# Kernel optimization log

Hardware: AMD Instinct MI355X
Metric: run time of the kernel (lower is better)

Reference implementation:

```python
import jax, jax.numpy as jnp
import numpy as np

D_MODEL = 1024
N_HEADS = 16
D_HEAD = D_MODEL // N_HEADS  # 64
D_FF = D_MODEL  # FeedForward(d_model, d_model) in source
B, S = 4, 1024
EPS = 1e-5


def layer_norm(x, gamma, beta):
    mu = jnp.mean(x, axis=-1, keepdims=True)
    var = jnp.mean(jnp.square(x - mu), axis=-1, keepdims=True)
    return (x - mu) * jax.lax.rsqrt(var + EPS) * gamma + beta


def setup_inputs() -> dict:
    key = jax.random.key(0)
    ks = jax.random.split(key, 16)
    s_embed = 1.0 / np.sqrt(D_MODEL)
    s_ff = 1.0 / np.sqrt(D_FF)
    return {
        "x": jax.random.normal(ks[0], (B, S, D_MODEL), jnp.float32),
        # per-head QKV projections stacked over heads: [H, d_embed, d_head]
        "Wq": jax.random.normal(ks[1], (N_HEADS, D_MODEL, D_HEAD), jnp.float32) * s_embed,
        "bq": jax.random.normal(ks[2], (N_HEADS, D_HEAD), jnp.float32) * s_embed,
        "Wk": jax.random.normal(ks[3], (N_HEADS, D_MODEL, D_HEAD), jnp.float32) * s_embed,
        "bk": jax.random.normal(ks[4], (N_HEADS, D_HEAD), jnp.float32) * s_embed,
        "Wv": jax.random.normal(ks[5], (N_HEADS, D_MODEL, D_HEAD), jnp.float32) * s_embed,
        "bv": jax.random.normal(ks[6], (N_HEADS, D_HEAD), jnp.float32) * s_embed,
        "Wo": jax.random.normal(ks[7], (D_MODEL, D_MODEL), jnp.float32) * s_embed,
        "bo": jax.random.normal(ks[8], (D_MODEL,), jnp.float32) * s_embed,
        "g1": jnp.ones((D_MODEL,), jnp.float32),
        "be1": jnp.zeros((D_MODEL,), jnp.float32),
        "W1": jax.random.normal(ks[9], (D_MODEL, D_FF), jnp.float32) * s_embed,
        "b1": jax.random.normal(ks[10], (D_FF,), jnp.float32) * s_embed,
        "W2": jax.random.normal(ks[11], (D_FF, D_MODEL), jnp.float32) * s_ff,
        "b2": jax.random.normal(ks[12], (D_MODEL,), jnp.float32) * s_ff,
        "g2": jnp.ones((D_MODEL,), jnp.float32),
        "be2": jnp.zeros((D_MODEL,), jnp.float32),
    }


def reference(x, Wq, bq, Wk, bk, Wv, bv, Wo, bo, g1, be1, W1, b1, W2, b2, g2, be2):
    scale = 1.0 / np.sqrt(D_HEAD).astype(np.float32)
    # batched per-head projections (equivalent to the per-head Linear loop)
    Q = jnp.einsum('bse,hed->bhsd', x, Wq) + bq[None, :, None, :]
    K = jnp.einsum('bse,hed->bhsd', x, Wk) + bk[None, :, None, :]
    V = jnp.einsum('bse,hed->bhsd', x, Wv) + bv[None, :, None, :]
    scores = jnp.einsum('bhsd,bhtd->bhst', Q, K) * scale
    attn = jax.nn.softmax(scores, axis=-1)
    ctx = jnp.einsum('bhst,bhtd->bhsd', attn, V)
    # concat heads along feature dim (head order matches the torch cat)
    ctx = jnp.transpose(ctx, (0, 2, 1, 3)).reshape(x.shape[0], x.shape[1], D_MODEL)
    attn_out = ctx @ Wo + bo
    y1 = layer_norm(x + attn_out, g1, be1)
    ff = jax.nn.relu(y1 @ W1 + b1) @ W2 + b2  # dropout is identity in eval
    return layer_norm(y1 + ff, g2, be2)
```

## Files before the change

kernel.cpp:

```cpp
#include <hip/hip_runtime.h>
#include <stdint.h>

#define BSZ 4
#define SEQ 1024
#define DM 1024
#define NH 16
#define DH 64
#define ROWS (BSZ * SEQ)
#define QS3 3072

typedef unsigned short u16;
typedef short bf16x8 __attribute__((ext_vector_type(8)));
typedef float f32x4 __attribute__((ext_vector_type(4)));

__device__ __forceinline__ float b2f(u16 u) {
    union { uint32_t i; float f; } v; v.i = ((uint32_t)u) << 16; return v.f;
}
__device__ __forceinline__ u16 f2b(float f) {
    union { float f; uint32_t i; } v; v.f = f;
    uint32_t u = v.i;
    return (u16)((u + 0x7FFFu + ((u >> 16) & 1u)) >> 16);
}
__device__ __forceinline__ u16 f2b_rh(float f) {
    union { float f; uint32_t i; } v; v.f = f;
    return (u16)((v.i + 0x8000u) >> 16);
}

__device__ __forceinline__ size_t blk_idx(int row, int col, int nkt) {
    return (((size_t)((row >> 7) * nkt + (col >> 5))) << 12)
         + ((((row >> 4) & 7) * 64 + ((col >> 3) & 3) * 16 + (row & 15)) << 3)
         + (col & 7);
}

typedef const __attribute__((address_space(1))) void gv_t;
typedef __attribute__((address_space(3))) void lv_t;
__device__ __forceinline__ void gl_lds16(const void* g, void* l) {
    __builtin_amdgcn_global_load_lds((gv_t*)g, (lv_t*)l, 16, 0, 0);
}

__global__ __launch_bounds__(256) void detect_dtype(
    const uint32_t* __restrict__ x, int* __restrict__ flag)
{
    __shared__ int red[256];
    const int tid = threadIdx.x;
    int sane = 0;
    for (int i = tid; i < 1024; i += 256) {
        uint32_t w = x[i];
        uint32_t lo = w & 0xFFFFu;
        uint32_t e = (lo >> 7) & 0xFF;
        if ((e >= 100 && e <= 140) || lo == 0) sane++;
    }
    red[tid] = sane;
    __syncthreads();
    for (int st = 128; st > 0; st >>= 1) {
        if (tid < st) red[tid] += red[tid + st];
        __syncthreads();
    }
    if (tid == 0) flag[0] = (red[0] < 512) ? 1 : 0;
}

__global__ __launch_bounds__(256) void convert_vecs(
    const void* bq, const void* bk, const void* bv, const void* bo,
    const void* b1, const void* b2, const void* g1, const void* be1,
    const void* g2, const void* be2, u16* __restrict__ dst,
    const int* __restrict__ flag)
{
    int i = blockIdx.x * 256 + threadIdx.x;
    int seg = i >> 10, off = i & 1023;
    const void* srcs[10] = {bq, bk, bv, bo, b1, b2, g1, be1, g2, be2};
    const void* s = srcs[seg];
    if (flag[0]) dst[i] = f2b(((const float*)s)[off]);
    else         dst[i] = ((const u16*)s)[off];
}

__global__ __launch_bounds__(256) void convert_x_blocked(
    const void* __restrict__ src, u16* __restrict__ dst,
    const int* __restrict__ flag)
{
    const int gid = blockIdx.x * 256 + threadIdx.x;
    const int tile = gid >> 9, c = gid & 511;
    const int p = tile >> 5, t = tile & 31;
    const int r = p * 128 + ((c >> 6) & 7) * 16 + (c & 15);
    const int k = t * 32 + ((c >> 4) & 3) * 8;
    union { uint4 q; u16 s[8]; } o;
    if (flag[0]) {
        const float* s = (const float*)src + (size_t)r * DM + k;
        float4 f0 = *(const float4*)s;
        float4 f1 = *(const float4*)(s + 4);
        o.s[0] = f2b(f0.x); o.s[1] = f2b(f0.y); o.s[2] = f2b(f0.z); o.s[3] = f2b(f0.w);
        o.s[4] = f2b(f1.x); o.s[5] = f2b(f1.y); o.s[6] = f2b(f1.z); o.s[7] = f2b(f1.w);
    } else {
        o.q = *(const uint4*)((const u16*)src + (size_t)r * DM + k);
    }
    *(uint4*)&dst[(size_t)gid * 8] = o.q;
}

__global__ __launch_bounds__(256) void transpose_blocked(
    const void* __restrict__ src, u16* __restrict__ dst, int R, int C,
    int n_off, const int* __restrict__ flag)
{
    __shared__ u16 Ts[32][33];
    const int tid = threadIdx.x;
    const int cb = blockIdx.x * 32, rb = blockIdx.y * 32, z = blockIdx.z;
    const int tr = tid >> 3, tc4 = (tid & 7) * 4;
    const size_t sbase = (size_t)z * R * C;

    u16 v[4];
    if (flag[0]) {
        const float* s = (const float*)src + sbase + (size_t)(rb + tr) * C + cb + tc4;
        float4 f = *(const float4*)s;
        v[0] = f2b(f.x); v[1] = f2b(f.y); v[2] = f2b(f.z); v[3] = f2b(f.w);
    } else {
        const u16* s = (const u16*)src + sbase + (size_t)(rb + tr) * C + cb + tc4;
        ushort4 f = *(const ushort4*)s;
        v[0] = f.x; v[1] = f.y; v[2] = f.z; v[3] = f.w;
    }
    #pragma unroll
    for (int j = 0; j < 4; ++j) Ts[tc4 + j][tr] = v[j];
    __syncthreads();

    if (tid < 128) {
        const int np = tid & 31, qp = tid >> 5;
        const int n = n_off + z * C + cb + np;
        const int k = rb + qp * 8;
        union { uint4 q; u16 s[8]; } o;
        #pragma unroll
        for (int j = 0; j < 8; ++j) o.s[j] = Ts[np][qp * 8 + j];
        *(uint4*)&dst[blk_idx(n, k, 32)] = o.q;
    }
}

__global__ __launch_bounds__(256) void gemm_b128(
    const u16* __restrict__ Ab, const u16* __restrict__ Bb,
    const u16* __restrict__ bias, const u16* __restrict__ resid,
    u16* __restrict__ C, int M, int N, int K,
    int relu, int c_blocked, int resid_blocked)
{
    __shared__ uint4 smem4[2176];
    u16* As = (u16*)smem4;
    u16* Bs = (u16*)smem4 + 8192;
    u16* Cs = (u16*)smem4;

    const int tid = threadIdx.x;
    const int w = tid >> 6, lane = tid & 63;
    const int l16 = lane & 15, quad = lane >> 4;
    const int wr = w >> 1, wc = w & 1;
    const int bm = blockIdx.y * 128, bn = blockIdx.x * 128;
    const int nkt = K >> 5;

    const u16* At = Ab + ((size_t)(bm >> 7) * nkt << 12);
    const u16* Bt = Bb + ((size_t)(bn >> 7) * nkt << 12);

    f32x4 acc[4][4];
    #pragma unroll
    for (int i = 0; i < 4; ++i)
        #pragma unroll
        for (int j = 0; j < 4; ++j)
            acc[i][j] = (f32x4){0.f, 0.f, 0.f, 0.f};

    const int co0 = (w * 64) * 8, co1 = (256 + w * 64) * 8;

    gl_lds16(&At[(size_t)0 + (w * 64 + lane) * 8],         &As[co0]);
    gl_lds16(&At[(size_t)0 + (256 + w * 64 + lane) * 8],   &As[co1]);
    gl_lds16(&Bt[(size_t)0 + (w * 64 + lane) * 8],         &Bs[co0]);
    gl_lds16(&Bt[(size_t)0 + (256 + w * 64 + lane) * 8],   &Bs[co1]);
    __syncthreads();

    for (int kt = 0; kt < nkt; ++kt) {
        const int cur = (kt & 1) * 4096, nxt = cur ^ 4096;
        if (kt + 1 < nkt) {
            const size_t tb = (size_t)(kt + 1) << 12;
            gl_lds16(&At[tb + (w * 64 + lane) * 8],       &As[nxt + co0]);
            gl_lds16(&At[tb + (256 + w * 64 + lane) * 8], &As[nxt + co1]);
            gl_lds16(&Bt[tb + (w * 64 + lane) * 8],       &Bs[nxt + co0]);
            gl_lds16(&Bt[tb + (256 + w * 64 + lane) * 8], &Bs[nxt + co1]);
        }

        bf16x8 a[4], b[4];
        #pragma unroll
        for (int i = 0; i < 4; ++i)
            a[i] = *(const bf16x8*)&As[cur + (((wr * 4 + i) * 64) + quad * 16 + l16) * 8];
        #pragma unroll
        for (int j = 0; j < 4; ++j)
            b[j] = *(const bf16x8*)&Bs[cur + (((wc * 4 + j) * 64) + quad * 16 + l16) * 8];

        #pragma unroll
        for (int i = 0; i < 4; ++i)
            #pragma unroll
            for (int j = 0; j < 4; ++j)
                acc[i][j] = __builtin_amdgcn_mfma_f32_16x16x32_bf16(a[i], b[j], acc[i][j], 0, 0, 0);
        __syncthreads();
    }

    #pragma unroll
    for (int j = 0; j < 4; ++j) {
        const int lc = wc * 64 + j * 16 + l16;
        const int col = bn + lc;
        const float bj = bias ? b2f(bias[col]) : 0.f;
        #pragma unroll
        for (int i = 0; i < 4; ++i) {
            #pragma unroll
            for (int r = 0; r < 4; ++r) {
                const int lr = wr * 64 + i * 16 + quad * 4 + r;
                float v = acc[i][j][r] + bj;
                if (resid) {
                    const size_t ri = resid_blocked ? blk_idx(bm + lr, col, N >> 5)
                                                    : (size_t)(bm + lr) * N + col;
                    v += b2f(resid[ri]);
                }
                if (relu) v = v > 0.f ? v : 0.f;
                Cs[lr * 136 + lc] = f2b(v);
            }
        }
    }
    __syncthreads();

    if (!c_blocked) {
        #pragma unroll
        for (int u = 0; u < 8; ++u) {
            const int g = u * 256 + tid;
            const int row = g >> 4, c16 = g & 15;
            uint4 val = *(const uint4*)&Cs[row * 136 + c16 * 8];
            *(uint4*)&C[(size_t)(bm + row) * N + bn + c16 * 8] = val;
        }
    } else {
        const size_t obase = ((size_t)((bm >> 7) * (N >> 5) + (bn >> 5))) << 12;
        #pragma unroll
        for (int u = 0; u < 8; ++u) {
            const int cc = u * 256 + tid;
            const int t2 = cc >> 9, c = cc & 511;
            const int row = ((c >> 6) & 7) * 16 + (c & 15);
            const int col = t2 * 32 + ((c >> 4) & 3) * 8;
            uint4 val = *(const uint4*)&Cs[row * 136 + col];
            *(uint4*)&C[obase + ((size_t)t2 << 12) + (size_t)c * 8] = val;
        }
    }
}

__global__ __launch_bounds__(256) void gemm_b64(
    const u16* __restrict__ Ab, const u16* __restrict__ Bb,
    const u16* __restrict__ bias, const u16* __restrict__ resid,
    u16* __restrict__ C, int M, int N, int K,
    int relu, int c_blocked, int resid_blocked)
{
    __shared__ uint4 smem4[1536];
    u16* As = (u16*)smem4;
    u16* Bs = (u16*)smem4 + 8192;
    u16* Cs = (u16*)smem4;

    const int tid = threadIdx.x;
    const int w = tid >> 6, lane = tid & 63;
    const int l16 = lane & 15, quad = lane >> 4;
    const int bm = blockIdx.y * 128, bn = blockIdx.x * 64;
    const int nkt = K >> 5;

    const u16* At = Ab + ((size_t)(bm >> 7) * nkt << 12);
    const int bsub = ((bn >> 6) & 1) * 256;
    const u16* Bt = Bb + ((size_t)(bn >> 7) * nkt << 12);

    f32x4 acc[2][4];
    #pragma unroll
    for (int i = 0; i < 2; ++i)
        #pragma unroll
        for (int j = 0; j < 4; ++j)
            acc[i][j] = (f32x4){0.f, 0.f, 0.f, 0.f};

    const int co0 = (w * 64) * 8, co1 = (256 + w * 64) * 8;

    gl_lds16(&At[(size_t)0 + (w * 64 + lane) * 8],       &As[co0]);
    gl_lds16(&At[(size_t)0 + (256 + w * 64 + lane) * 8], &As[co1]);
    gl_lds16(&Bt[(size_t)0 + (bsub + w * 64 + lane) * 8], &Bs[co0]);
    __syncthreads();

    for (int kt = 0; kt < nkt; ++kt) {
        const int curA = (kt & 1) * 4096, nxtA = curA ^ 4096;
        const int curB = (kt & 1) * 2048, nxtB = curB ^ 2048;
        if (kt + 1 < nkt) {
            const size_t tb = (size_t)(kt + 1) << 12;
            gl_lds16(&At[tb + (w * 64 + lane) * 8],        &As[nxtA + co0]);
            gl_lds16(&At[tb + (256 + w * 64 + lane) * 8],  &As[nxtA + co1]);
            gl_lds16(&Bt[tb + (bsub + w * 64 + lane) * 8], &Bs[nxtB + co0]);
        }

        bf16x8 a[2], b[4];
        #pragma unroll
        for (int i = 0; i < 2; ++i)
            a[i] = *(const bf16x8*)&As[curA + (((w * 2 + i) * 64) + quad * 16 + l16) * 8];
        #pragma unroll
        for (int j = 0; j < 4; ++j)
            b[j] = *(const bf16x8*)&Bs[curB + ((j * 64) + quad * 16 + l16) * 8];

        #pragma unroll
        for (int i = 0; i < 2; ++i)
            #pragma unroll
            for (int j = 0; j < 4; ++j)
                acc[i][j] = __builtin_amdgcn_mfma_f32_16x16x32_bf16(a[i], b[j], acc[i][j], 0, 0, 0);
        __syncthreads();
    }

    #pragma unroll
    for (int j = 0; j < 4; ++j) {
        const int lc = j * 16 + l16;
        const int col = bn + lc;
        const float bj = bias ? b2f(bias[col]) : 0.f;
        #pragma unroll
        for (int i = 0; i < 2; ++i) {
            #pragma unroll
            for (int r = 0; r < 4; ++r) {
                const int lr = w * 32 + i * 16 + quad * 4 + r;
                float v = acc[i][j][r] + bj;
                if (resid) {
                    const size_t ri = resid_blocked ? blk_idx(bm + lr, col, N >> 5)
                                                    : (size_t)(bm + lr) * N + col;
                    v += b2f(resid[ri]);
                }
                if (relu) v = v > 0.f ? v : 0.f;
                Cs[lr * 72 + lc] = f2b(v);
            }
        }
    }
    __syncthreads();

    if (!c_blocked) {
        #pragma unroll
        for (int u = 0; u < 4; ++u) {
            const int g = u * 256 + tid;
            const int row = g >> 3, c16 = g & 7;
            uint4 val = *(const uint4*)&Cs[row * 72 + c16 * 8];
            *(uint4*)&C[(size_t)(bm + row) * N + bn + c16 * 8] = val;
        }
    } else {
        const size_t obase = ((size_t)((bm >> 7) * (N >> 5) + (bn >> 5))) << 12;
        #pragma unroll
        for (int u = 0; u < 4; ++u) {
            const int cc = u * 256 + tid;
            const int t2 = cc >> 9, c = cc & 511;
            const int row = ((c >> 6) & 7) * 16 + (c & 15);
            const int col = t2 * 32 + ((c >> 4) & 3) * 8;
            uint4 val = *(const uint4*)&Cs[row * 72 + col];
            *(uint4*)&C[obase + ((size_t)t2 << 12) + (size_t)c * 8] = val;
        }
    }
}

__global__ __launch_bounds__(512) void attn_mfma(
    const u16* __restrict__ QKV, u16* __restrict__ ctx)
{
    __shared__ u16 Qf[8192];
    __shared__ u16 Kf[2][4096];
    __shared__ u16 VtT[2][64 * 72];
    __shared__ u16 Ps[8 * 16 * 72];

    const int qt = blockIdx.x, h = blockIdx.y, b = blockIdx.z;
    const int tid = threadIdx.x;
    const int w = tid >> 6, lane = tid & 63;
    const int l16 = lane & 15, quad = lane >> 4;
    const size_t qrow0 = (size_t)(b * SEQ + qt * 128);
    const size_t brow = (size_t)(b * SEQ);
    const int hoff = h * DH;

    const size_t qg = (qrow0 + w * 16 + l16) * QS3 + hoff + quad * 8;
    gl_lds16(&QKV[qg],      &Qf[w * 1024]);
    gl_lds16(&QKV[qg + 32], &Qf[w * 1024 + 512]);

    const int kt_ = w >> 1, kh_ = w & 1;
    const size_t kgbase = (size_t)(kt_ * 16 + l16) * QS3 + 1024 + hoff + kh_ * 32 + quad * 8;
    const int kdst = kt_ * 1024 + kh_ * 512;

    const int vk2 = (tid & 31) * 2, vd0 = (tid >> 5) * 4;
    const size_t vgbase = (size_t)vk2 * QS3 + 2048 + hoff + vd0;

    gl_lds16(&QKV[brow * QS3 + kgbase], &Kf[0][kdst]);
    {
        uint2 a0 = *(const uint2*)&QKV[brow * QS3 + vgbase];
        uint2 a1 = *(const uint2*)&QKV[brow * QS3 + vgbase + QS3];
        uint32_t w0 = (a0.x & 0xFFFFu) | (a1.x << 16);
        uint32_t w1 = (a0.x >> 16)     | (a1.x & 0xFFFF0000u);
        uint32_t w2 = (a0.y & 0xFFFFu) | (a1.y << 16);
        uint32_t w3 = (a0.y >> 16)     | (a1.y & 0xFFFF0000u);
        *(uint32_t*)&VtT[0][(vd0 + 0) * 72 + vk2] = w0;
        *(uint32_t*)&VtT[0][(vd0 + 1) * 72 + vk2] = w1;
        *(uint32_t*)&VtT[0][(vd0 + 2) * 72 + vk2] = w2;
        *(uint32_t*)&VtT[0][(vd0 + 3) * 72 + vk2] = w3;
    }
    __syncthreads();

    bf16x8 aQ0 = *(const bf16x8*)&Qf[w * 1024 +       lane * 8];
    bf16x8 aQ1 = *(const bf16x8*)&Qf[w * 1024 + 512 + lane * 8];

    f32x4 O[4];
    #pragma unroll
    for (int dt = 0; dt < 4; ++dt) O[dt] = (f32x4){0.f, 0.f, 0.f, 0.f};
    float lacc[4] = {0.f, 0.f, 0.f, 0.f};

    for (int kt64 = 0; kt64 < SEQ / 64; ++kt64) {
        const int cur = kt64 & 1, nxt = cur ^ 1;
        uint2 a0, a1;
        const bool more = (kt64 + 1 < SEQ / 64);
        if (more) {
            const size_t krow = brow + (size_t)(kt64 + 1) * 64;
            gl_lds16(&QKV[krow * QS3 + kgbase], &Kf[nxt][kdst]);
            a0 = *(const uint2*)&QKV[krow * QS3 + vgbase];
            a1 = *(const uint2*)&QKV[krow * QS3 + vgbase + QS3];
        }

        f32x4 St[4];
        #pragma unroll
        for (int t = 0; t < 4; ++t) {
            bf16x8 b0 = *(const bf16x8*)&Kf[cur][t * 1024 +       lane * 8];
            bf16x8 b1 = *(const bf16x8*)&Kf[cur][t * 1024 + 512 + lane * 8];
            f32x4 z = (f32x4){0.f, 0.f, 0.f, 0.f};
            z = __builtin_amdgcn_mfma_f32_16x16x32_bf16(aQ0, b0, z, 0, 0, 0);
            z = __builtin_amdgcn_mfma_f32_16x16x32_bf16(aQ1, b1, z, 0, 0, 0);
            St[t] = z;
        }

        #pragma unroll
        for (int t = 0; t < 4; ++t)
            #pragma unroll
            for (int r = 0; r < 4; ++r) {
                const float p = __expf(St[t][r] * 0.125f);
                lacc[r] += p;
                Ps[w * 1152 + (quad * 4 + r) * 72 + t * 16 + l16] = f2b_rh(p);
            }

        bf16x8 aP0 = *(const bf16x8*)&Ps[w * 1152 + l16 * 72 +  0 + quad * 8];
        bf16x8 aP1 = *(const bf16x8*)&Ps[w * 1152 + l16 * 72 + 32 + quad * 8];
        #pragma unroll
        for (int dt = 0; dt < 4; ++dt) {
            bf16x8 vv0 = *(const bf16x8*)&VtT[cur][(dt * 16 + l16) * 72 +  0 + quad * 8];
            bf16x8 vv1 = *(const bf16x8*)&VtT[cur][(dt * 16 + l16) * 72 + 32 + quad * 8];
            O[dt] = __builtin_amdgcn_mfma_f32_16x16x32_bf16(aP0, vv0, O[dt], 0, 0, 0);
            O[dt] = __builtin_amdgcn_mfma_f32_16x16x32_bf16(aP1, vv1, O[dt], 0, 0, 0);
        }

        if (more) {
            uint32_t w0 = (a0.x & 0xFFFFu) | (a1.x << 16);
            uint32_t w1 = (a0.x >> 16)     | (a1.x & 0xFFFF0000u);
            uint32_t w2 = (a0.y & 0xFFFFu) | (a1.y << 16);
            uint32_t w3 = (a0.y >> 16)     | (a1.y & 0xFFFF0000u);
            *(uint32_t*)&VtT[nxt][(vd0 + 0) * 72 + vk2] = w0;
            *(uint32_t*)&VtT[nxt][(vd0 + 1) * 72 + vk2] = w1;
            *(uint32_t*)&VtT[nxt][(vd0 + 2) * 72 + vk2] = w2;
            *(uint32_t*)&VtT[nxt][(vd0 + 3) * 72 + vk2] = w3;
        }
        __syncthreads();
    }

    const size_t pbase = ((size_t)(qrow0 >> 7) * 32) << 12;
    #pragma unroll
    for (int r = 0; r < 4; ++r) {
        float s = lacc[r];
        s += __shfl_xor(s, 1);
        s += __shfl_xor(s, 2);
        s += __shfl_xor(s, 4);
        s += __shfl_xor(s, 8);
        const float inv = 1.0f / s;
        #pragma unroll
        for (int dt = 0; dt < 4; ++dt) {
            const int t = h * 2 + (dt >> 1);
            const int q = (dt & 1) * 2 + (l16 >> 3);
            const size_t idx = pbase + ((size_t)t << 12)
                             + ((w * 64 + q * 16 + quad * 4 + r) << 3) + (l16 & 7);
            ctx[idx] = f2b(O[dt][r] * inv);
        }
    }
}

__global__ __launch_bounds__(256) void layernorm_kernel(
    const u16* __restrict__ X, const u16* __restrict__ gamma,
    const u16* __restrict__ beta, void* __restrict__ Y,
    const int* __restrict__ flag, int y_mode)
{
    __shared__ float red[256], red2[256];
    const int r = blockIdx.x, tid = threadIdx.x;
    const u16* xp = X + (size_t)r * DM;

    ushort4 v = *(const ushort4*)(xp + tid * 4);
    float x0 = b2f(v.x), x1 = b2f(v.y), x2 = b2f(v.z), x3 = b2f(v.w);
    red[tid]  = x0 + x1 + x2 + x3;
    red2[tid] = x0 * x0 + x1 * x1 + x2 * x2 + x3 * x3;
    __syncthreads();
    for (int st = 128; st > 0; st >>= 1) {
        if (tid < st) { red[tid] += red[tid + st]; red2[tid] += red2[tid + st]; }
        __syncthreads();
    }
    const float mu = red[0] * (1.0f / DM);
    const float var = red2[0] * (1.0f / DM) - mu * mu;
    const float rstd = rsqrtf(var + 1e-5f);

    ushort4 g = *(const ushort4*)(gamma + tid * 4);
    ushort4 be = *(const ushort4*)(beta + tid * 4);
    float y0 = (x0 - mu) * rstd * b2f(g.x) + b2f(be.x);
    float y1 = (x1 - mu) * rstd * b2f(g.y) + b2f(be.y);
    float y2 = (x2 - mu) * rstd * b2f(g.z) + b2f(be.z);
    float y3 = (x3 - mu) * rstd * b2f(g.w) + b2f(be.w);

    const int k = tid * 4;
    if (y_mode == 2 && flag[0]) {
        float* yp = (float*)Y + (size_t)r * DM + k;
        yp[0] = y0; yp[1] = y1; yp[2] = y2; yp[3] = y3;
    } else if (y_mode == 1) {
        u16* yp = (u16*)Y + blk_idx(r, k, 32);
        ushort4 o; o.x = f2b(y0); o.y = f2b(y1); o.z = f2b(y2); o.w = f2b(y3);
        *(ushort4*)yp = o;
    } else {
        u16* yp = (u16*)Y + (size_t)r * DM + k;
        ushort4 o; o.x = f2b(y0); o.y = f2b(y1); o.z = f2b(y2); o.w = f2b(y3);
        *(ushort4*)yp = o;
    }
}

extern "C" void kernel_launch(void* const* d_in, const int* in_sizes, int n_in,
                              void* d_out, int out_size, void* d_ws, size_t ws_size,
                              hipStream_t stream) {
    const void* x_raw   = d_in[0];
    const void* Wq_raw  = d_in[1];
    const void* bq_raw  = d_in[2];
    const void* Wk_raw  = d_in[3];
    const void* bk_raw  = d_in[4];
    const void* Wv_raw  = d_in[5];
    const void* bv_raw  = d_in[6];
    const void* Wo_raw  = d_in[7];
    const void* bo_raw  = d_in[8];
    const void* g1_raw  = d_in[9];
    const void* be1_raw = d_in[10];
    const void* W1_raw  = d_in[11];
    const void* b1_raw  = d_in[12];
    const void* W2_raw  = d_in[13];
    const void* b2_raw  = d_in[14];
    const void* g2_raw  = d_in[15];
    const void* be2_raw = d_in[16];

    char* ws = (char*)d_ws;
    const size_t MB = 1024 * 1024;
    int* flag   = (int*)ws;
    u16* x_b    = (u16*)(ws + 1 * MB);
    u16* WqkvB  = (u16*)(ws + 9 * MB);
    u16* WoB    = (u16*)(ws + 15 * MB);
    u16* W1B    = (u16*)(ws + 17 * MB);
    u16* W2B    = (u16*)(ws + 19 * MB);
    u16* vecs   = (u16*)(ws + 21 * MB);
    u16* bqkv_c = vecs;
    u16* bo_c   = vecs + 3072;
    u16* b1_c   = vecs + 4096;
    u16* b2_c   = vecs + 5120;
    u16* g1_c   = vecs + 6144;
    u16* be1_c  = vecs + 7168;
    u16* g2_c   = vecs + 8192;
    u16* be2_c  = vecs + 9216;
    u16* QKVb   = (u16*)(ws + 22 * MB);
    u16* y1B    = QKVb;
    u16* hmidB  = QKVb + 4 * MB;
    u16* ctxB   = (u16*)(ws + 48 * MB);
    u16* res1   = (u16*)(ws + 56 * MB);
    u16* res2   = res1;

    detect_dtype<<<1, 256, 0, stream>>>((const uint32_t*)x_raw, flag);

    convert_x_blocked<<<2048, 256, 0, stream>>>(x_raw, x_b, flag);

    dim3 gt_qkv(2, 32, NH);
    transpose_blocked<<<gt_qkv, 256, 0, stream>>>(Wq_raw, WqkvB, DM, DH,    0, flag);
    transpose_blocked<<<gt_qkv, 256, 0, stream>>>(Wk_raw, WqkvB, DM, DH, 1024, flag);
    transpose_blocked<<<gt_qkv, 256, 0, stream>>>(Wv_raw, WqkvB, DM, DH, 2048, flag);
    dim3 gt_sq(32, 32, 1);
    transpose_blocked<<<gt_sq, 256, 0, stream>>>(Wo_raw, WoB, DM, DM, 0, flag);
    transpose_blocked<<<gt_sq, 256, 0, stream>>>(W1_raw, W1B, DM, DM, 0, flag);
    transpose_blocked<<<gt_sq, 256, 0, stream>>>(W2_raw, W2B, DM, DM, 0, flag);

    convert_vecs<<<40, 256, 0, stream>>>(bq_raw, bk_raw, bv_raw, bo_raw,
                                         b1_raw, b2_raw, g1_raw, be1_raw,
                                         g2_raw, be2_raw, vecs, flag);

    gemm_b128<<<dim3(QS3 / 128, ROWS / 128), 256, 0, stream>>>(
        x_b, WqkvB, bqkv_c, nullptr, QKVb, ROWS, QS3, DM, 0, 0, 0);

    attn_mfma<<<dim3(SEQ / 128, NH, BSZ), 512, 0, stream>>>(QKVb, ctxB);

    dim3 gg64(DM / 64, ROWS / 128);
    gemm_b64<<<gg64, 256, 0, stream>>>(ctxB, WoB, bo_c, x_b, res1, ROWS, DM, DM, 0, 0, 1);
    layernorm_kernel<<<ROWS, 256, 0, stream>>>(res1, g1_c, be1_c, (void*)y1B, flag, 1);
    gemm_b64<<<gg64, 256, 0, stream>>>(y1B, W1B, b1_c, nullptr, hmidB, ROWS, DM, DM, 1, 1, 0);
    gemm_b64<<<gg64, 256, 0, stream>>>(hmidB, W2B, b2_c, y1B, res2, ROWS, DM, DM, 0, 0, 1);
    layernorm_kernel<<<ROWS, 256, 0, stream>>>(res2, g2_c, be2_c, d_out, flag, 2);
}
```

Before: 277.5 us.

## Write QKV in attention-ready blocked layouts and merge prep kernels into one launch

The QKV GEMM epilogue now writes Q, K and V straight into per-head blocked layouts, with V pre-transposed, so the attention kernel can stage K and V tiles into LDS with direct global-to-LDS copies. This removes the in-kernel V transpose and the strided row loads. The dtype conversion, weight transpose and vector conversion kernels are also merged into a single prep_all launch to cut launch overhead. In exchange the GEMM epilogue does scattered LDS reads for the V transpose, and the attention context output indexing changes.

```diff
diff --git a/kernel.cpp b/kernel.cpp
--- a/kernel.cpp
+++ b/kernel.cpp
@@ -59,54 +59,70 @@
     if (tid == 0) flag[0] = (red[0] < 512) ? 1 : 0;
 }
 
-__global__ __launch_bounds__(256) void convert_vecs(
+__global__ __launch_bounds__(256) void prep_all(
+    const void* x_raw, const void* Wq, const void* Wk, const void* Wv,
+    const void* Wo, const void* W1, const void* W2,
     const void* bq, const void* bk, const void* bv, const void* bo,
     const void* b1, const void* b2, const void* g1, const void* be1,
-    const void* g2, const void* be2, u16* __restrict__ dst,
+    const void* g2, const void* be2,
+    u16* __restrict__ x_b, u16* __restrict__ WqkvB, u16* __restrict__ WoB,
+    u16* __restrict__ W1B, u16* __restrict__ W2B, u16* __restrict__ vecs,
     const int* __restrict__ flag)
 {
-    int i = blockIdx.x * 256 + threadIdx.x;
-    int seg = i >> 10, off = i & 1023;
-    const void* srcs[10] = {bq, bk, bv, bo, b1, b2, g1, be1, g2, be2};
-    const void* s = srcs[seg];
-    if (flag[0]) dst[i] = f2b(((const float*)s)[off]);
-    else         dst[i] = ((const u16*)s)[off];
-}
-
-__global__ __launch_bounds__(256) void convert_x_blocked(
-    const void* __restrict__ src, u16* __restrict__ dst,
-    const int* __restrict__ flag)
-{
-    const int gid = blockIdx.x * 256 + threadIdx.x;
-    const int tile = gid >> 9, c = gid & 511;
-    const int p = tile >> 5, t = tile & 31;
-    const int r = p * 128 + ((c >> 6) & 7) * 16 + (c & 15);
-    const int k = t * 32 + ((c >> 4) & 3) * 8;
-    union { uint4 q; u16 s[8]; } o;
-    if (flag[0]) {
-        const float* s = (const float*)src + (size_t)r * DM + k;
-        float4 f0 = *(const float4*)s;
-        float4 f1 = *(const float4*)(s + 4);
-        o.s[0] = f2b(f0.x); o.s[1] = f2b(f0.y); o.s[2] = f2b(f0.z); o.s[3] = f2b(f0.w);
-        o.s[4] = f2b(f1.x); o.s[5] = f2b(f1.y); o.s[6] = f2b(f1.z); o.s[7] = f2b(f1.w);
+    const int bid = blockIdx.x, tid = threadIdx.x;
+    const int isf = flag[0];
+
+    if (bid < 2048) {
+        const int gid = bid * 256 + tid;
+        const int tile = gid >> 9, c = gid & 511;
+        const int p = tile >> 5, t = tile & 31;
+        const int r = p * 128 + ((c >> 6) & 7) * 16 + (c & 15);
+        const int k = t * 32 + ((c >> 4) & 3) * 8;
+        union { uint4 q; u16 s[8]; } o;
+        if (isf) {
+            const float* s = (const float*)x_raw + (size_t)r * DM + k;
+            float4 f0 = *(const float4*)s;
+            float4 f1 = *(const float4*)(s + 4);
+            o.s[0] = f2b(f0.x); o.s[1] = f2b(f0.y); o.s[2] = f2b(f0.z); o.s[3] = f2b(f0.w);
+            o.s[4] = f2b(f1.x); o.s[5] = f2b(f1.y); o.s[6] = f2b(f1.z); o.s[7] = f2b(f1.w);
+        } else {
+            o.q = *(const uint4*)((const u16*)x_raw + (size_t)r * DM + k);
+        }
+        *(uint4*)&x_b[(size_t)gid * 8] = o.q;
+        return;
+    }
+    if (bid >= 8192) {
+        const int i = (bid - 8192) * 256 + tid;
+        const int seg = i >> 10, off = i & 1023;
+        const void* srcs[10] = {bq, bk, bv, bo, b1, b2, g1, be1, g2, be2};
+        const void* s = srcs[seg];
+        vecs[i] = isf ? f2b(((const float*)s)[off]) : ((const u16*)s)[off];
+        return;
+    }
+
+    const void* src; u16* dst; int R, C, n_off, bx, by, z;
+    if (bid < 5120) {
+        const int which = (bid - 2048) >> 10;
+        const int lb = (bid - 2048) & 1023;
+        src = which == 0 ? Wq : (which == 1 ? Wk : Wv);
+        dst = WqkvB; R = DM; C = DH; n_off = which * 1024;
+        bx = lb & 1; by = (lb >> 1) & 31; z = lb >> 6;
     } else {
-        o.q = *(const uint4*)((const u16*)src + (size_t)r * DM + k);
-    }
-    *(uint4*)&dst[(size_t)gid * 8] = o.q;
-}
-
-__global__ __launch_bounds__(256) void transpose_blocked(
-    const void* __restrict__ src, u16* __restrict__ dst, int R, int C,
-    int n_off, const int* __restrict__ flag)
-{
+        const int which = (bid - 5120) >> 10;
+        const int lb = (bid - 5120) & 1023;
+        src = which == 0 ? Wo : (which == 1 ? W1 : W2);
+        dst = which == 0 ? WoB : (which == 1 ? W1B : W2B);
+        R = DM; C = DM; n_off = 0;
+        bx = lb & 31; by = (lb >> 5) & 31; z = 0;
+    }
+
     __shared__ u16 Ts[32][33];
-    const int tid = threadIdx.x;
-    const int cb = blockIdx.x * 32, rb = blockIdx.y * 32, z = blockIdx.z;
+    const int cb = bx * 32, rb = by * 32;
     const int tr = tid >> 3, tc4 = (tid & 7) * 4;
     const size_t sbase = (size_t)z * R * C;
 
     u16 v[4];
-    if (flag[0]) {
+    if (isf) {
         const float* s = (const float*)src + sbase + (size_t)(rb + tr) * C + cb + tc4;
         float4 f = *(const float4*)s;
         v[0] = f2b(f.x); v[1] = f2b(f.y); v[2] = f2b(f.z); v[3] = f2b(f.w);
@@ -130,11 +146,10 @@
     }
 }
 
-__global__ __launch_bounds__(256) void gemm_b128(
+__global__ __launch_bounds__(256) void gemm_qkv(
     const u16* __restrict__ Ab, const u16* __restrict__ Bb,
-    const u16* __restrict__ bias, const u16* __restrict__ resid,
-    u16* __restrict__ C, int M, int N, int K,
-    int relu, int c_blocked, int resid_blocked)
+    const u16* __restrict__ bias,
+    u16* __restrict__ Qblk, u16* __restrict__ Kblk, u16* __restrict__ Vblk)
 {
     __shared__ uint4 smem4[2176];
     u16* As = (u16*)smem4;
@@ -146,7 +161,7 @@
     const int l16 = lane & 15, quad = lane >> 4;
     const int wr = w >> 1, wc = w & 1;
     const int bm = blockIdx.y * 128, bn = blockIdx.x * 128;
-    const int nkt = K >> 5;
+    const int nkt = 32;
 
     const u16* At = Ab + ((size_t)(bm >> 7) * nkt << 12);
     const u16* Bt = Bb + ((size_t)(bn >> 7) * nkt << 12);
@@ -160,10 +175,10 @@
 
     const int co0 = (w * 64) * 8, co1 = (256 + w * 64) * 8;
 
-    gl_lds16(&At[(size_t)0 + (w * 64 + lane) * 8],         &As[co0]);
-    gl_lds16(&At[(size_t)0 + (256 + w * 64 + lane) * 8],   &As[co1]);
-    gl_lds16(&Bt[(size_t)0 + (w * 64 + lane) * 8],         &Bs[co0]);
-    gl_lds16(&Bt[(size_t)0 + (256 + w * 64 + lane) * 8],   &Bs[co1]);
+    gl_lds16(&At[(w * 64 + lane) * 8],         &As[co0]);
+    gl_lds16(&At[(256 + w * 64 + lane) * 8],   &As[co1]);
+    gl_lds16(&Bt[(w * 64 + lane) * 8],         &Bs[co0]);
+    gl_lds16(&Bt[(256 + w * 64 + lane) * 8],   &Bs[co1]);
     __syncthreads();
 
     for (int kt = 0; kt < nkt; ++kt) {
@@ -195,44 +210,50 @@
     #pragma unroll
     for (int j = 0; j < 4; ++j) {
         const int lc = wc * 64 + j * 16 + l16;
-        const int col = bn + lc;
-        const float bj = bias ? b2f(bias[col]) : 0.f;
-        #pragma unroll
-        for (int i = 0; i < 4; ++i) {
+        const float bj = b2f(bias[bn + lc]);
+        #pragma unroll
+        for (int i = 0; i < 4; ++i)
             #pragma unroll
             for (int r = 0; r < 4; ++r) {
                 const int lr = wr * 64 + i * 16 + quad * 4 + r;
-                float v = acc[i][j][r] + bj;
-                if (resid) {
-                    const size_t ri = resid_blocked ? blk_idx(bm + lr, col, N >> 5)
-                                                    : (size_t)(bm + lr) * N + col;
-                    v += b2f(resid[ri]);
-                }
-                if (relu) v = v > 0.f ? v : 0.f;
-                Cs[lr * 136 + lc] = f2b(v);
+                Cs[lr * 136 + lc] = f2b(acc[i][j][r] + bj);
             }
-        }
-    }
-    __syncthreads();
-
-    if (!c_blocked) {
+    }
+    __syncthreads();
+
+    const int b_ = bm >> 10, sb16 = (bm & 1023) >> 4, kb64 = (bm & 1023) >> 6;
+    if (bn < 2048) {
+        u16* out = (bn < 1024) ? Qblk : Kblk;
+        const int hbase = (bn & 1023) >> 6;
         #pragma unroll
         for (int u = 0; u < 8; ++u) {
             const int g = u * 256 + tid;
-            const int row = g >> 4, c16 = g & 15;
-            uint4 val = *(const uint4*)&Cs[row * 136 + c16 * 8];
-            *(uint4*)&C[(size_t)(bm + row) * N + bn + c16 * 8] = val;
+            const int hh = g >> 10, rem = g & 1023;
+            const int s16r = rem >> 7, rem2 = rem & 127;
+            const int half = rem2 >> 6, lam = rem2 & 63;
+            const int row = s16r * 16 + (lam & 15);
+            const int col = hh * 64 + half * 32 + (lam >> 4) * 8;
+            uint4 val = *(const uint4*)&Cs[row * 136 + col];
+            const size_t gi = ((size_t)((b_ * 16 + hbase + hh) * 64 + sb16 + s16r)) * 1024
+                            + half * 512 + (size_t)lam * 8;
+            *(uint4*)&out[gi] = val;
         }
     } else {
-        const size_t obase = ((size_t)((bm >> 7) * (N >> 5) + (bn >> 5))) << 12;
+        const int hbase = (bn - 2048) >> 6;
         #pragma unroll
         for (int u = 0; u < 8; ++u) {
-            const int cc = u * 256 + tid;
-            const int t2 = cc >> 9, c = cc & 511;
-            const int row = ((c >> 6) & 7) * 16 + (c & 15);
-            const int col = t2 * 32 + ((c >> 4) & 3) * 8;
-            uint4 val = *(const uint4*)&Cs[row * 136 + col];
-            *(uint4*)&C[obase + ((size_t)t2 << 12) + (size_t)c * 8] = val;
+            const int g = u * 256 + tid;
+            const int hh = g >> 10, rem = g & 1023;
+            const int kt64r = rem >> 9, dt = (rem >> 7) & 3;
+            const int half = (rem >> 6) & 1, lam = rem & 63;
+            const int d = dt * 16 + (lam & 15);
+            const int s0 = kt64r * 64 + half * 32 + (lam >> 4) * 8;
+            union { uint4 q; u16 s[8]; } o;
+            #pragma unroll
+            for (int j = 0; j < 8; ++j) o.s[j] = Cs[(s0 + j) * 136 + hh * 64 + d];
+            const size_t gi = ((size_t)((b_ * 16 + hbase + hh) * 16 + kb64 + kt64r)) * 4096
+                            + dt * 1024 + half * 512 + (size_t)lam * 8;
+            *(uint4*)&Vblk[gi] = o.q;
         }
     }
 }
@@ -267,9 +288,9 @@
 
     const int co0 = (w * 64) * 8, co1 = (256 + w * 64) * 8;
 
-    gl_lds16(&At[(size_t)0 + (w * 64 + lane) * 8],       &As[co0]);
-    gl_lds16(&At[(size_t)0 + (256 + w * 64 + lane) * 8], &As[co1]);
-    gl_lds16(&Bt[(size_t)0 + (bsub + w * 64 + lane) * 8], &Bs[co0]);
+    gl_lds16(&At[(w * 64 + lane) * 8],        &As[co0]);
+    gl_lds16(&At[(256 + w * 64 + lane) * 8],  &As[co1]);
+    gl_lds16(&Bt[(bsub + w * 64 + lane) * 8], &Bs[co0]);
     __syncthreads();
 
     for (int kt = 0; kt < nkt; ++kt) {
@@ -344,11 +365,12 @@
 }
 
 __global__ __launch_bounds__(512) void attn_mfma(
-    const u16* __restrict__ QKV, u16* __restrict__ ctx)
+    const u16* __restrict__ Qblk, const u16* __restrict__ Kblk,
+    const u16* __restrict__ Vblk, u16* __restrict__ ctx)
 {
     __shared__ u16 Qf[8192];
     __shared__ u16 Kf[2][4096];
-    __shared__ u16 VtT[2][64 * 72];
+    __shared__ u16 Vf[2][4096];
     __shared__ u16 Ps[8 * 16 * 72];
 
     const int qt = blockIdx.x, h = blockIdx.y, b = blockIdx.z;
@@ -356,33 +378,18 @@
     const int w = tid >> 6, lane = tid & 63;
     const int l16 = lane & 15, quad = lane >> 4;
     const size_t qrow0 = (size_t)(b * SEQ + qt * 128);
-    const size_t brow = (size_t)(b * SEQ);
+    const int bh = b * NH + h;
     const int hoff = h * DH;
 
-    const size_t qg = (qrow0 + w * 16 + l16) * QS3 + hoff + quad * 8;
-    gl_lds16(&QKV[qg],      &Qf[w * 1024]);
-    gl_lds16(&QKV[qg + 32], &Qf[w * 1024 + 512]);
-
-    const int kt_ = w >> 1, kh_ = w & 1;
-    const size_t kgbase = (size_t)(kt_ * 16 + l16) * QS3 + 1024 + hoff + kh_ * 32 + quad * 8;
-    const int kdst = kt_ * 1024 + kh_ * 512;
-
-    const int vk2 = (tid & 31) * 2, vd0 = (tid >> 5) * 4;
-    const size_t vgbase = (size_t)vk2 * QS3 + 2048 + hoff + vd0;
-
-    gl_lds16(&QKV[brow * QS3 + kgbase], &Kf[0][kdst]);
-    {
-        uint2 a0 = *(const uint2*)&QKV[brow * QS3 + vgbase];
-        uint2 a1 = *(const uint2*)&QKV[brow * QS3 + vgbase + QS3];
-        uint32_t w0 = (a0.x & 0xFFFFu) | (a1.x << 16);
-        uint32_t w1 = (a0.x >> 16)     | (a1.x & 0xFFFF0000u);
-        uint32_t w2 = (a0.y & 0xFFFFu) | (a1.y << 16);
-        uint32_t w3 = (a0.y >> 16)     | (a1.y & 0xFFFF0000u);
-        *(uint32_t*)&VtT[0][(vd0 + 0) * 72 + vk2] = w0;
-        *(uint32_t*)&VtT[0][(vd0 + 1) * 72 + vk2] = w1;
-        *(uint32_t*)&VtT[0][(vd0 + 2) * 72 + vk2] = w2;
-        *(uint32_t*)&VtT[0][(vd0 + 3) * 72 + vk2] = w3;
-    }
+    const u16* Qg = Qblk + ((size_t)(bh * 64 + qt * 8 + w)) * 1024 + (size_t)lane * 8;
+    gl_lds16(Qg,       &Qf[w * 1024]);
+    gl_lds16(Qg + 512, &Qf[w * 1024 + 512]);
+
+    const u16* Kg = Kblk + ((size_t)(bh * 64)) * 1024 + (size_t)w * 512 + (size_t)lane * 8;
+    const u16* Vg = Vblk + ((size_t)(bh * 16)) * 4096 + (size_t)w * 512 + (size_t)lane * 8;
+
+    gl_lds16(Kg, &Kf[0][w * 512]);
+    gl_lds16(Vg, &Vf[0][w * 512]);
     __syncthreads();
 
     bf16x8 aQ0 = *(const bf16x8*)&Qf[w * 1024 +       lane * 8];
@@ -395,13 +402,9 @@
 
     for (int kt64 = 0; kt64 < SEQ / 64; ++kt64) {
         const int cur = kt64 & 1, nxt = cur ^ 1;
-        uint2 a0, a1;
-        const bool more = (kt64 + 1 < SEQ / 64);
-        if (more) {
-            const size_t krow = brow + (size_t)(kt64 + 1) * 64;
-            gl_lds16(&QKV[krow * QS3 + kgbase], &Kf[nxt][kdst]);
-            a0 = *(const uint2*)&QKV[krow * QS3 + vgbase];
-            a1 = *(const uint2*)&QKV[krow * QS3 + vgbase + QS3];
+        if (kt64 + 1 < SEQ / 64) {
+            gl_lds16(Kg + (size_t)(kt64 + 1) * 4096, &Kf[nxt][w * 512]);
+            gl_lds16(Vg + (size_t)(kt64 + 1) * 4096, &Vf[nxt][w * 512]);
         }
 
         f32x4 St[4];
@@ -428,21 +431,10 @@
         bf16x8 aP1 = *(const bf16x8*)&Ps[w * 1152 + l16 * 72 + 32 + quad * 8];
         #pragma unroll
         for (int dt = 0; dt < 4; ++dt) {
-            bf16x8 vv0 = *(const bf16x8*)&VtT[cur][(dt * 16 + l16) * 72 +  0 + quad * 8];
-            bf16x8 vv1 = *(const bf16x8*)&VtT[cur][(dt * 16 + l16) * 72 + 32 + quad * 8];
+            bf16x8 vv0 = *(const bf16x8*)&Vf[cur][dt * 1024 +       lane * 8];
+            bf16x8 vv1 = *(const bf16x8*)&Vf[cur][dt * 1024 + 512 + lane * 8];
             O[dt] = __builtin_amdgcn_mfma_f32_16x16x32_bf16(aP0, vv0, O[dt], 0, 0, 0);
             O[dt] = __builtin_amdgcn_mfma_f32_16x16x32_bf16(aP1, vv1, O[dt], 0, 0, 0);
-        }
-
-        if (more) {
-            uint32_t w0 = (a0.x & 0xFFFFu) | (a1.x << 16);
-            uint32_t w1 = (a0.x >> 16)     | (a1.x & 0xFFFF0000u);
-            uint32_t w2 = (a0.y & 0xFFFFu) | (a1.y << 16);
-            uint32_t w3 = (a0.y >> 16)     | (a1.y & 0xFFFF0000u);
-            *(uint32_t*)&VtT[nxt][(vd0 + 0) * 72 + vk2] = w0;
-            *(uint32_t*)&VtT[nxt][(vd0 + 1) * 72 + vk2] = w1;
-            *(uint32_t*)&VtT[nxt][(vd0 + 2) * 72 + vk2] = w2;
-            *(uint32_t*)&VtT[nxt][(vd0 + 3) * 72 + vk2] = w3;
         }
         __syncthreads();
     }
@@ -458,11 +450,12 @@
         const float inv = 1.0f / s;
         #pragma unroll
         for (int dt = 0; dt < 4; ++dt) {
-            const int t = h * 2 + (dt >> 1);
-            const int q = (dt & 1) * 2 + (l16 >> 3);
+            const int t = (hoff + dt * 16) >> 5;
+            const int q = (((hoff + dt * 16) >> 3) & 3);
             const size_t idx = pbase + ((size_t)t << 12)
                              + ((w * 64 + q * 16 + quad * 4 + r) << 3) + (l16 & 7);
-            ctx[idx] = f2b(O[dt][r] * inv);
+            const size_t idx2 = idx + (((size_t)(l16 >> 3)) << 7);
+            ctx[idx2] = f2b(O[dt][r] * inv);
         }
     }
 }
@@ -549,34 +542,27 @@
     u16* be1_c  = vecs + 7168;
     u16* g2_c   = vecs + 8192;
     u16* be2_c  = vecs + 9216;
-    u16* QKVb   = (u16*)(ws + 22 * MB);
-    u16* y1B    = QKVb;
-    u16* hmidB  = QKVb + 4 * MB;
+    u16* Qblk   = (u16*)(ws + 22 * MB);
+    u16* Kblk   = (u16*)(ws + 30 * MB);
+    u16* Vblk   = (u16*)(ws + 38 * MB);
     u16* ctxB   = (u16*)(ws + 48 * MB);
     u16* res1   = (u16*)(ws + 56 * MB);
+    u16* y1B    = Qblk;
+    u16* hmidB  = Kblk;
     u16* res2   = res1;
 
     detect_dtype<<<1, 256, 0, stream>>>((const uint32_t*)x_raw, flag);
 
-    convert_x_blocked<<<2048, 256, 0, stream>>>(x_raw, x_b, flag);
-
-    dim3 gt_qkv(2, 32, NH);
-    transpose_blocked<<<gt_qkv, 256, 0, stream>>>(Wq_raw, WqkvB, DM, DH,    0, flag);
-    transpose_blocked<<<gt_qkv, 256, 0, stream>>>(Wk_raw, WqkvB, DM, DH, 1024, flag);
-    transpose_blocked<<<gt_qkv, 256, 0, stream>>>(Wv_raw, WqkvB, DM, DH, 2048, flag);
-    dim3 gt_sq(32, 32, 1);
-    transpose_blocked<<<gt_sq, 256, 0, stream>>>(Wo_raw, WoB, DM, DM, 0, flag);
-    transpose_blocked<<<gt_sq, 256, 0, stream>>>(W1_raw, W1B, DM, DM, 0, flag);
-    transpose_blocked<<<gt_sq, 256, 0, stream>>>(W2_raw, W2B, DM, DM, 0, flag);
-
-    convert_vecs<<<40, 256, 0, stream>>>(bq_raw, bk_raw, bv_raw, bo_raw,
-                                         b1_raw, b2_raw, g1_raw, be1_raw,
-                                         g2_raw, be2_raw, vecs, flag);
-
-    gemm_b128<<<dim3(QS3 / 128, ROWS / 128), 256, 0, stream>>>(
-        x_b, WqkvB, bqkv_c, nullptr, QKVb, ROWS, QS3, DM, 0, 0, 0);
-
-    attn_mfma<<<dim3(SEQ / 128, NH, BSZ), 512, 0, stream>>>(QKVb, ctxB);
+    prep_all<<<8232, 256, 0, stream>>>(
+        x_raw, Wq_raw, Wk_raw, Wv_raw, Wo_raw, W1_raw, W2_raw,
+        bq_raw, bk_raw, bv_raw, bo_raw, b1_raw, b2_raw,
+        g1_raw, be1_raw, g2_raw, be2_raw,
+        x_b, WqkvB, WoB, W1B, W2B, vecs, flag);
+
+    gemm_qkv<<<dim3(QS3 / 128, ROWS / 128), 256, 0, stream>>>(
+        x_b, WqkvB, bqkv_c, Qblk, Kblk, Vblk);
+
+    attn_mfma<<<dim3(SEQ / 128, NH, BSZ), 512, 0, stream>>>(Qblk, Kblk, Vblk, ctxB);
 
     dim3 gg64(DM / 64, ROWS / 128);
     gemm_b64<<<gg64, 256, 0, stream>>>(ctxB, WoB, bo_c, x_b, res1, ROWS, DM, DM, 0, 0, 1);
```

Result: faster. 267.1 us (-3.7%).
